# Performance work log

Measured on AMD Instinct MI355X. Metric: run time of the kernel, lower is better.

The kernel has to match this reference:

```python
import jax, jax.numpy as jnp
import numpy as np

B, N, E = 4, 8192, 131072
R, NUM_CLASSES, H, OUT = 16, 100, 128, 32


def _rgcn_layer(h, W, src, dst, rel, mask_edge):
    # h: [B,N,in], W: [R,in,out], src/dst/rel: [B,E] int, mask_edge: [B,E]
    # Per-edge msg = h[src] @ W[rel] * norm(=1); computed as per-relation
    # projection of all nodes followed by a (src, rel) gather.
    proj = jnp.einsum('bni,rio->bnro', h, W)          # [B,N,R,out]
    bidx = jnp.arange(B)[:, None]                      # [B,1]
    msg = proj[bidx, src, rel] * mask_edge[..., None]  # [B,E,out]
    # scatter-sum messages onto destination nodes (fn.sum in DGL)
    seg = (jnp.arange(B)[:, None] * N + dst).reshape(-1)
    out = jax.ops.segment_sum(msg.reshape(B * E, -1), seg, num_segments=B * N)
    return out.reshape(B, N, -1)


def setup_inputs() -> dict:
    key = jax.random.key(0)
    ks = jax.random.split(key, 10)
    class_objects = jax.random.randint(ks[0], (B, N), 0, NUM_CLASSES)
    states_objects = jax.random.normal(ks[1], (B, N, 8), dtype=jnp.float32)
    edge_tuples = jax.random.randint(ks[2], (B, E, 2), 0, N)
    edge_classes = jax.random.randint(ks[3], (B, E), 0, R)
    mask_object = jnp.ones((B, N), dtype=jnp.float32)
    mask_edge = jnp.ones((B, E), dtype=jnp.float32)
    embed = jax.random.normal(ks[4], (NUM_CLASSES, H), dtype=jnp.float32) * 0.05
    W1 = jax.random.normal(ks[5], (R, H, H), dtype=jnp.float32) * 0.05
    W2 = jax.random.normal(ks[6], (R, H, H), dtype=jnp.float32) * 0.05
    W3 = jax.random.normal(ks[7], (R, H, OUT), dtype=jnp.float32) * 0.05
    return {'class_objects': class_objects, 'states_objects': states_objects,
            'edge_tuples': edge_tuples, 'edge_classes': edge_classes,
            'mask_object': mask_object, 'mask_edge': mask_edge,
            'embed': embed, 'W1': W1, 'W2': W2, 'W3': W3}


def reference(class_objects, states_objects, edge_tuples, edge_classes,
              mask_object, mask_edge, embed, W1, W2, W3):
    src = edge_tuples[..., 0]
    dst = edge_tuples[..., 1]
    rel = edge_classes
    h = embed[class_objects]                                  # [B,N,H]
    h = jax.nn.relu(_rgcn_layer(h, W1, src, dst, rel, mask_edge))
    h = jax.nn.relu(_rgcn_layer(h, W2, src, dst, rel, mask_edge))
    h = jax.nn.softmax(_rgcn_layer(h, W3, src, dst, rel, mask_edge), axis=-1)
    # original pads each env's node features with zeros up to max_nodes
    return h * mask_object[..., None]                         # [B,N,OUT]
```

## Files before the change

kernel.cpp:

```cpp
#include <hip/hip_runtime.h>

typedef __attribute__((ext_vector_type(4))) float f32x4;
typedef __attribute__((ext_vector_type(8))) short short8;

#define B_ 4
#define N_ 8192
#define E_ 131072
#define R_ 16
#define H_ 128
#define OUT_ 32
#define NKEYS (B_*N_*R_)
#define NEDGE (B_*E_)
#define NEXT_MASK 0x7FFFFu

__device__ __forceinline__ unsigned short f2bf(float f){
  unsigned int u = __float_as_uint(f);
  u = (u + 0x7fffu + ((u>>16)&1u)) >> 16;
  return (unsigned short)u;
}
__device__ __forceinline__ float bfh(unsigned u, int hi){
  return __uint_as_float(hi ? (u & 0xffff0000u) : (u << 16));
}
__device__ __forceinline__ unsigned cvtpk(float lo, float hi){
  unsigned r;
  asm("v_cvt_pk_bf16_f32 %0, %1, %2" : "=v"(r) : "v"(lo), "v"(hi));
  return r;
}
__device__ __forceinline__ void glds16(const void* g, void* l){
  __builtin_amdgcn_global_load_lds((const __attribute__((address_space(1))) unsigned int*)g,
                                   (__attribute__((address_space(3))) unsigned int*)l,
                                   16, 0, 0);
}


__global__ void link_k(const int* __restrict__ et, const int* __restrict__ ec,
                       int* __restrict__ head, unsigned* __restrict__ link){
  int e = blockIdx.x*256 + threadIdx.x;
  int b = e >> 17;
  int2 sd = *(const int2*)(et + 2*e);
  int r  = ec[e];
  int key = (((b<<13)+sd.y)<<4) + r;
  int old = atomicExch(&head[key], e);
  unsigned nxt = (old < 0) ? (unsigned)e : (unsigned)old;
  link[e] = (((unsigned)sd.x) << 19) | nxt;
}


__global__ void cmap_k(const int* __restrict__ head, const unsigned* __restrict__ link,
                       const float* __restrict__ me,
                       int* __restrict__ cmapA, int* __restrict__ cmapB,
                       int hARow, int hBRow, int aggcRow){
  int key = blockIdx.x*256 + threadIdx.x;
  int hd = head[key];
  int vA = aggcRow, vB = aggcRow;
  if (hd >= 0) {
    unsigned lk = link[hd];
    int nxt = (int)(lk & NEXT_MASK);
    if (nxt == hd && me[hd] == 1.0f) {
      int noderow = ((key >> 17) << 13) + (int)(lk >> 19);
      vA = hARow + noderow;
      vB = hBRow + noderow;
    } else {
      vA = aggcRow + 1 + key;
      vB = vA;
    }
  }
  cmapA[key] = vA;
  cmapB[key] = vB;
}


__global__ void prep_k(const int* __restrict__ cls, const float* __restrict__ emb,
                       const float* __restrict__ W1, const float* __restrict__ W2,
                       const float* __restrict__ W3,
                       unsigned short* __restrict__ h,
                       unsigned short* __restrict__ W1t,
                       unsigned short* __restrict__ W2t,
                       unsigned short* __restrict__ W3t,
                       unsigned short* __restrict__ aggc){
  int t = blockIdx.x*256 + threadIdx.x;
  if (blockIdx.x == 0 && threadIdx.x < 16) {
    *(uint4*)((char*)aggc + threadIdx.x*16) = make_uint4(0,0,0,0);
  }
  if (t < B_*N_*32) {
    int node = t>>5, c = t&31;
    int cl = cls[node];
    float4 v = *(const float4*)(emb + cl*H_ + c*4);
    uint2 o;
    o.x = f2bf(v.x) | ((unsigned int)f2bf(v.y)<<16);
    o.y = f2bf(v.z) | ((unsigned int)f2bf(v.w)<<16);
    *(uint2*)(h + node*H_ + c*4) = o;
  } else {
    int u = t - B_*N_*32;
    if (u < R_*H_*H_) {
      int k = u & 127, n = (u>>7) & 127, r = u >> 14;
      W1t[u] = f2bf(W1[(r*H_ + k)*H_ + n]);
    } else if (u < 2*R_*H_*H_) {
      int u2 = u - R_*H_*H_;
      int k = u2 & 127, n = (u2>>7) & 127, r = u2 >> 14;
      W2t[u2] = f2bf(W2[(r*H_ + k)*H_ + n]);
    } else {
      int u2 = u - 2*R_*H_*H_;
      if (u2 < R_*OUT_*H_) {
        int k = u2 & 127, n = (u2>>7) & 31, r = u2 >> 12;
        W3t[u2] = f2bf(W3[(r*H_ + k)*OUT_ + n]);
      }
    }
  }
}


__global__ __launch_bounds__(256) void agg_k(
    const unsigned short* __restrict__ h_in,
    const int* __restrict__ head,
    const unsigned* __restrict__ link,
    const float* __restrict__ me,
    unsigned short* __restrict__ aggc){
  const int orig = blockIdx.x;
  const int x    = orig & 7;
  const int b    = x >> 1;
  const int lb   = ((x & 1) << 10) + (orig >> 3);
  const int key  = (b << 17) + (lb << 6) + (threadIdx.x >> 2);
  const int q    = threadIdx.x & 3;
  int hd = head[key];
  if (hd < 0) return;
  unsigned lk = link[hd];
  int nxt = (int)(lk & NEXT_MASK);
  float m0 = me[hd];
  if (nxt == hd && m0 == 1.0f) return;
  const unsigned short* hb = h_in + ((size_t)b << 20);

  float fa[32];
  #pragma unroll
  for (int i=0;i<32;++i) fa[i] = 0.f;

#define UNP8(FP, V, M) do { \
  (FP)[0]+=M*bfh((V).x,0); (FP)[1]+=M*bfh((V).x,1); \
  (FP)[2]+=M*bfh((V).y,0); (FP)[3]+=M*bfh((V).y,1); \
  (FP)[4]+=M*bfh((V).z,0); (FP)[5]+=M*bfh((V).z,1); \
  (FP)[6]+=M*bfh((V).w,0); (FP)[7]+=M*bfh((V).w,1); \
} while(0)
#define MAC32(SRC, M) do { \
  const uint4* hp_ = (const uint4*)(hb + (((unsigned)(SRC))<<7) + (q<<5)); \
  uint4 v0_ = hp_[0], v1_ = hp_[1], v2_ = hp_[2], v3_ = hp_[3]; \
  UNP8(fa+0,  v0_, M); UNP8(fa+8,  v1_, M); \
  UNP8(fa+16, v2_, M); UNP8(fa+24, v3_, M); \
} while(0)

  int cur = hd;
  unsigned clk = lk;
  float cm = m0;
  for (;;) {
    int src = (int)(clk >> 19);
    MAC32(src, cm);
    int nx = (int)(clk & NEXT_MASK);
    if (nx == cur) break;
    cur = nx;
    clk = link[cur];
    cm  = me[cur];
  }
#undef MAC32
#undef UNP8

  unsigned short* ap = aggc + (((size_t)(1 + key)) << 7) + (q<<5);
  #pragma unroll
  for (int c = 0; c < 4; ++c) {
    uint4 pk;
    pk.x = cvtpk(fa[c*8+0], fa[c*8+1]);
    pk.y = cvtpk(fa[c*8+2], fa[c*8+3]);
    pk.z = cvtpk(fa[c*8+4], fa[c*8+5]);
    pk.w = cvtpk(fa[c*8+6], fa[c*8+7]);
    *(uint4*)(ap + c*8) = pk;
  }
}


template<int NOUT>
__global__ __launch_bounds__((NOUT==128) ? 1024 : 512, 4) void gemm_k(
    const unsigned short* __restrict__ base,
    const int* __restrict__ cmap,
    const unsigned short* __restrict__ Wt,
    const float* __restrict__ mobj,
    unsigned short* __restrict__ h_out,
    float* __restrict__ out)
{
  constexpr int MT  = (NOUT==128) ? 128 : 64;
  constexpr int MI  = (NOUT==128) ? 2 : 1;
  constexpr int NIw = (NOUT==128) ? 2 : 1;
  __shared__ __align__(16) unsigned short A_s[3][MT*64];
  __shared__ __align__(16) unsigned short B_s[3][NOUT*64];
  __shared__ int cmap_s[MT*16];
  __shared__ float comb[(NOUT==32) ? 64*33 : 1];

  const int tid  = threadIdx.x;
  const int lane = tid & 63;
  const int w    = tid >> 6;
  const int c16  = lane & 15;
  const int g    = lane >> 4;
  const int m0   = blockIdx.x * MT;
  const int mbase = (NOUT==128) ? ((w>>2)<<5) : ((w>>1)<<4);
  const int nbase = (NOUT==128) ? ((w&3)<<5) : ((w&1)<<4);

  *(int2*)&cmap_s[tid<<1] = *(const int2*)(cmap + m0*16 + (tid<<1));
  __syncthreads();

#define STAGE(KC, BUF) do { \
  const int kc_ = (KC); \
  { \
    int m_ = tid>>3, u_ = tid&7; \
    int cm_ = cmap_s[(m_<<4) + (kc_>>1)]; \
    glds16((const char*)base + ((size_t)cm_<<8) + ((kc_&1)<<7) + ((u_ ^ (m_&7))<<4), \
           &A_s[BUF][tid<<3]); \
  } \
  if constexpr (NOUT==128) { \
    int n_ = tid>>3, u_ = tid&7; \
    glds16((const char*)Wt + ((size_t)((kc_>>1)*128 + n_)<<8) + ((kc_&1)<<7) + ((u_ ^ (n_&7))<<4), \
           &B_s[BUF][tid<<3]); \
  } else { \
    if (w < 4) { \
      int uid_ = (w<<6) + lane; \
      int n_ = uid_>>3, u_ = uid_&7; \
      glds16((const char*)Wt + ((size_t)((kc_>>1)*32 + n_)<<8) + ((kc_&1)<<7) + ((u_ ^ (n_&7))<<4), \
             &B_s[BUF][uid_<<3]); } \
  } \
} while(0)

#define WAIT_MAIN do { \
  if constexpr (NOUT==128) { asm volatile("s_waitcnt vmcnt(4)" ::: "memory"); } \
  else { if (w < 4) asm volatile("s_waitcnt vmcnt(4)" ::: "memory"); \
         else       asm volatile("s_waitcnt vmcnt(2)" ::: "memory"); } \
} while(0)
#define WAIT_T1 do { \
  if constexpr (NOUT==128) { asm volatile("s_waitcnt vmcnt(2)" ::: "memory"); } \
  else { if (w < 4) asm volatile("s_waitcnt vmcnt(2)" ::: "memory"); \
         else       asm volatile("s_waitcnt vmcnt(1)" ::: "memory"); } \
} while(0)

  f32x4 acc[MI][NIw];
  #pragma unroll
  for (int mi=0; mi<MI; ++mi)
    #pragma unroll
    for (int ni=0; ni<NIw; ++ni)
      acc[mi][ni] = f32x4{0.f,0.f,0.f,0.f};

#define COMPUTE(BUF) do { \
  _Pragma("unroll") \
  for (int kk=0; kk<2; ++kk) { \
    short8 af[MI], bfr[NIw]; \
    _Pragma("unroll") \
    for (int mi=0; mi<MI; ++mi) { \
      int m_ = mbase + mi*16 + c16; \
      af[mi] = *(const short8*)((const char*)&A_s[BUF][0] + m_*128 \
               + (((kk<<6) + (g<<4)) ^ ((m_&7)<<4))); } \
    _Pragma("unroll") \
    for (int ni=0; ni<NIw; ++ni) { \
      int n_ = nbase + ni*16 + c16; \
      bfr[ni] = *(const short8*)((const char*)&B_s[BUF][0] + n_*128 \
               + (((kk<<6) + (g<<4)) ^ ((n_&7)<<4))); } \
    _Pragma("unroll") \
    for (int mi=0; mi<MI; ++mi) \
      _Pragma("unroll") \
      for (int ni=0; ni<NIw; ++ni) \
        acc[mi][ni] = __builtin_amdgcn_mfma_f32_16x16x32_bf16(af[mi], bfr[ni], acc[mi][ni], 0,0,0); \
  } \
} while(0)

  STAGE(0, 0);
  STAGE(1, 1);
  for (int kc = 0; kc < 30; ++kc) {
    STAGE(kc+2, (kc+2)%3);
    WAIT_MAIN;
    __builtin_amdgcn_s_barrier();
    COMPUTE(kc%3);
    asm volatile("s_waitcnt lgkmcnt(0)" ::: "memory");
    __builtin_amdgcn_s_barrier();
  }
  WAIT_T1;
  __builtin_amdgcn_s_barrier();
  COMPUTE(0);
  asm volatile("s_waitcnt lgkmcnt(0)" ::: "memory");
  __builtin_amdgcn_s_barrier();
  asm volatile("s_waitcnt vmcnt(0)" ::: "memory");
  __builtin_amdgcn_s_barrier();
  COMPUTE(1);

  if constexpr (NOUT == 128) {
    #pragma unroll
    for (int mi=0; mi<MI; ++mi)
      #pragma unroll
      for (int ni=0; ni<NIw; ++ni)
        #pragma unroll
        for (int j=0; j<4; ++j) {
          int row = mbase + mi*16 + (g<<2) + j;
          int col = nbase + ni*16 + c16;
          h_out[((size_t)(m0+row)<<7) + col] = f2bf(fmaxf(acc[mi][ni][j], 0.f));
        }
  } else {
    #pragma unroll
    for (int j=0; j<4; ++j)
      comb[(mbase + (g<<2) + j)*33 + nbase + c16] = acc[0][0][j];
    __syncthreads();
    if (tid < 64) {
      const int row = tid;
      float v[32];
      #pragma unroll
      for (int c=0; c<32; ++c) v[c] = comb[row*33 + c];
      float mx = v[0];
      #pragma unroll
      for (int c=1; c<32; ++c) mx = fmaxf(mx, v[c]);
      float sm = 0.f;
      #pragma unroll
      for (int c=0; c<32; ++c){ v[c] = __expf(v[c]-mx); sm += v[c]; }
      float sc = mobj[m0+row] / sm;
      float4* op = (float4*)(out + ((size_t)(m0+row)<<5));
      #pragma unroll
      for (int c=0; c<8; ++c)
        op[c] = make_float4(v[4*c]*sc, v[4*c+1]*sc, v[4*c+2]*sc, v[4*c+3]*sc);
    }
  }
#undef STAGE
#undef WAIT_MAIN
#undef WAIT_T1
#undef COMPUTE
}

extern "C" void kernel_launch(void* const* d_in, const int* in_sizes, int n_in,
                              void* d_out, int out_size, void* d_ws, size_t ws_size,
                              hipStream_t stream){
  const int*   cls   = (const int*)  d_in[0];
  const int*   et    = (const int*)  d_in[2];
  const int*   ec    = (const int*)  d_in[3];
  const float* mobj  = (const float*)d_in[4];
  const float* medge = (const float*)d_in[5];
  const float* emb   = (const float*)d_in[6];
  const float* W1    = (const float*)d_in[7];
  const float* W2    = (const float*)d_in[8];
  const float* W3    = (const float*)d_in[9];
  float* out = (float*)d_out;

  char* ws = (char*)d_ws;
  size_t o = 0;
  auto alloc = [&](size_t bytes)->char*{
    char* p = ws + o;
    o += (bytes + 255) & ~(size_t)255;
    return p;
  };
  unsigned short* hA    = (unsigned short*)alloc((size_t)B_*N_*H_*2);
  unsigned short* hB    = (unsigned short*)alloc((size_t)B_*N_*H_*2);
  unsigned short* W1t   = (unsigned short*)alloc((size_t)R_*H_*H_*2);
  unsigned short* W2t   = (unsigned short*)alloc((size_t)R_*H_*H_*2);
  unsigned short* W3t   = (unsigned short*)alloc((size_t)R_*OUT_*H_*2);
  int*            head  = (int*)alloc((size_t)NKEYS*4);
  unsigned*       link  = (unsigned*)alloc((size_t)NEDGE*4);
  int*            cmapA = (int*)alloc((size_t)NKEYS*4);
  int*            cmapB = (int*)alloc((size_t)NKEYS*4);
  unsigned short* aggc  = (unsigned short*)alloc(((size_t)NKEYS+1)*H_*2);
  (void)ws_size; (void)in_sizes; (void)n_in; (void)out_size;

  const int hARow   = (int)(((char*)hA   - ws) >> 8);
  const int hBRow   = (int)(((char*)hB   - ws) >> 8);
  const int aggcRow = (int)(((char*)aggc - ws) >> 8);
  const unsigned short* vbase = (const unsigned short*)ws;

  hipMemsetAsync(head, 0xFF, (size_t)NKEYS*4, stream);
  hipLaunchKernelGGL(link_k, dim3(NEDGE/256), dim3(256), 0, stream, et, ec, head, link);
  hipLaunchKernelGGL(cmap_k, dim3(NKEYS/256), dim3(256), 0, stream, head, link, medge,
                     cmapA, cmapB, hARow, hBRow, aggcRow);

  hipLaunchKernelGGL(prep_k, dim3((B_*N_*32 + 2*R_*H_*H_ + R_*OUT_*H_)/256), dim3(256), 0, stream,
                     cls, emb, W1, W2, W3, hA, W1t, W2t, W3t, aggc);

  const int aggGrid = (NKEYS*4)/256;
  const int g128    = (B_*N_)/128;
  const int g32     = (B_*N_)/64;

  hipLaunchKernelGGL(agg_k, dim3(aggGrid), dim3(256), 0, stream, hA, head, link, medge, aggc);
  hipLaunchKernelGGL((gemm_k<128>), dim3(g128), dim3(1024), 0, stream,
                     vbase, cmapA, W1t, (const float*)nullptr, hB, (float*)nullptr);
  hipLaunchKernelGGL(agg_k, dim3(aggGrid), dim3(256), 0, stream, hB, head, link, medge, aggc);
  hipLaunchKernelGGL((gemm_k<128>), dim3(g128), dim3(1024), 0, stream,
                     vbase, cmapB, W2t, (const float*)nullptr, hA, (float*)nullptr);
  hipLaunchKernelGGL(agg_k, dim3(aggGrid), dim3(256), 0, stream, hA, head, link, medge, aggc);
  hipLaunchKernelGGL((gemm_k<32>), dim3(g32), dim3(512), 0, stream,
                     vbase, cmapA, W3t, mobj, (unsigned short*)nullptr, out);
}
```

Baseline: 207.2 us.

## Precompute per-class embedding×W1 table and fuse layer one into edge gather

Layer one's input is an embedding lookup, so each message depends only on the (relation, class) pair. The new code precomputes a 16×100×128 fp32 table of emb·W1[r] and has each node walk its incoming edge lists, summing table rows with relu and bf16 packing fused in. This removes the first aggregation kernel, the first GEMM and the embedding materialisation. In exchange there are serial per-thread linked-list walks with scattered table reads, and accumulation stays in fp32 without the bf16 rounding of h and W1 that the old path applied.

```diff
diff --git a/kernel.cpp b/kernel.cpp
--- a/kernel.cpp
+++ b/kernel.cpp
@@ -9,6 +9,7 @@
 #define R_ 16
 #define H_ 128
 #define OUT_ 32
+#define NCLS 100
 #define NKEYS (B_*N_*R_)
 #define NEDGE (B_*E_)
 #define NEXT_MASK 0x7FFFFu
@@ -70,42 +71,88 @@
 }
 
 
-__global__ void prep_k(const int* __restrict__ cls, const float* __restrict__ emb,
-                       const float* __restrict__ W1, const float* __restrict__ W2,
-                       const float* __restrict__ W3,
-                       unsigned short* __restrict__ h,
-                       unsigned short* __restrict__ W1t,
+__global__ void prep_k(const float* __restrict__ W2, const float* __restrict__ W3,
                        unsigned short* __restrict__ W2t,
                        unsigned short* __restrict__ W3t,
                        unsigned short* __restrict__ aggc){
-  int t = blockIdx.x*256 + threadIdx.x;
+  int u = blockIdx.x*256 + threadIdx.x;
   if (blockIdx.x == 0 && threadIdx.x < 16) {
     *(uint4*)((char*)aggc + threadIdx.x*16) = make_uint4(0,0,0,0);
   }
-  if (t < B_*N_*32) {
-    int node = t>>5, c = t&31;
-    int cl = cls[node];
-    float4 v = *(const float4*)(emb + cl*H_ + c*4);
-    uint2 o;
-    o.x = f2bf(v.x) | ((unsigned int)f2bf(v.y)<<16);
-    o.y = f2bf(v.z) | ((unsigned int)f2bf(v.w)<<16);
-    *(uint2*)(h + node*H_ + c*4) = o;
+  if (u < R_*H_*H_) {
+    int k = u & 127, n = (u>>7) & 127, r = u >> 14;
+    W2t[u] = f2bf(W2[(r*H_ + k)*H_ + n]);
   } else {
-    int u = t - B_*N_*32;
-    if (u < R_*H_*H_) {
-      int k = u & 127, n = (u>>7) & 127, r = u >> 14;
-      W1t[u] = f2bf(W1[(r*H_ + k)*H_ + n]);
-    } else if (u < 2*R_*H_*H_) {
-      int u2 = u - R_*H_*H_;
-      int k = u2 & 127, n = (u2>>7) & 127, r = u2 >> 14;
-      W2t[u2] = f2bf(W2[(r*H_ + k)*H_ + n]);
-    } else {
-      int u2 = u - 2*R_*H_*H_;
-      if (u2 < R_*OUT_*H_) {
-        int k = u2 & 127, n = (u2>>7) & 31, r = u2 >> 12;
-        W3t[u2] = f2bf(W3[(r*H_ + k)*OUT_ + n]);
+    int u2 = u - R_*H_*H_;
+    if (u2 < R_*OUT_*H_) {
+      int k = u2 & 127, n = (u2>>7) & 31, r = u2 >> 12;
+      W3t[u2] = f2bf(W3[(r*H_ + k)*OUT_ + n]);
+    }
+  }
+}
+
+
+__global__ void embw_k(const float* __restrict__ emb, const float* __restrict__ W1,
+                       float* __restrict__ embW1){
+  int t = blockIdx.x*256 + threadIdx.x;
+  int n  = t & 127;
+  int cl = (t >> 7) % NCLS;
+  int r  = t / (NCLS*H_);
+  const float* er = emb + cl*H_;
+  const float* wr = W1 + (size_t)r*H_*H_;
+  float s = 0.f;
+  #pragma unroll 4
+  for (int k = 0; k < H_; ++k)
+    s += er[k] * wr[k*H_ + n];
+  embW1[t] = s;
+}
+
+
+__global__ __launch_bounds__(256) void layer1_k(
+    const int* __restrict__ cls, const float* __restrict__ embW1,
+    const int* __restrict__ head, const unsigned* __restrict__ link,
+    const float* __restrict__ me,
+    unsigned short* __restrict__ h1){
+  int t = blockIdx.x*256 + threadIdx.x;
+  int node = t >> 2;
+  int q = t & 3;
+  const int b = node >> 13;
+  const int* clsb = cls + (b << 13);
+
+  float fa[32];
+  #pragma unroll
+  for (int i=0;i<32;++i) fa[i] = 0.f;
+
+  for (int r = 0; r < R_; ++r) {
+    int cur = head[(node<<4) + r];
+    if (cur < 0) continue;
+    for (;;) {
+      unsigned lk = link[cur];
+      float m = me[cur];
+      int src = (int)(lk >> 19);
+      int cl = clsb[src];
+      const float4* tp = (const float4*)(embW1 + ((r*NCLS + cl) << 7) + (q<<5));
+      #pragma unroll
+      for (int c = 0; c < 8; ++c) {
+        float4 v = tp[c];
+        fa[c*4+0] += m*v.x; fa[c*4+1] += m*v.y;
+        fa[c*4+2] += m*v.z; fa[c*4+3] += m*v.w;
       }
+      int nx = (int)(lk & NEXT_MASK);
+      if (nx == cur) break;
+      cur = nx;
     }
+  }
+
+  unsigned short* op = h1 + ((size_t)node << 7) + (q<<5);
+  #pragma unroll
+  for (int c = 0; c < 4; ++c) {
+    uint4 pk;
+    pk.x = cvtpk(fmaxf(fa[c*8+0],0.f), fmaxf(fa[c*8+1],0.f));
+    pk.y = cvtpk(fmaxf(fa[c*8+2],0.f), fmaxf(fa[c*8+3],0.f));
+    pk.z = cvtpk(fmaxf(fa[c*8+4],0.f), fmaxf(fa[c*8+5],0.f));
+    pk.w = cvtpk(fmaxf(fa[c*8+6],0.f), fmaxf(fa[c*8+7],0.f));
+    *(uint4*)(op + c*8) = pk;
   }
 }
 
@@ -347,7 +394,7 @@
   };
   unsigned short* hA    = (unsigned short*)alloc((size_t)B_*N_*H_*2);
   unsigned short* hB    = (unsigned short*)alloc((size_t)B_*N_*H_*2);
-  unsigned short* W1t   = (unsigned short*)alloc((size_t)R_*H_*H_*2);
+  float*          embW1 = (float*)alloc((size_t)R_*NCLS*H_*4);
   unsigned short* W2t   = (unsigned short*)alloc((size_t)R_*H_*H_*2);
   unsigned short* W3t   = (unsigned short*)alloc((size_t)R_*OUT_*H_*2);
   int*            head  = (int*)alloc((size_t)NKEYS*4);
@@ -367,16 +414,16 @@
   hipLaunchKernelGGL(cmap_k, dim3(NKEYS/256), dim3(256), 0, stream, head, link, medge,
                      cmapA, cmapB, hARow, hBRow, aggcRow);
 
-  hipLaunchKernelGGL(prep_k, dim3((B_*N_*32 + 2*R_*H_*H_ + R_*OUT_*H_)/256), dim3(256), 0, stream,
-                     cls, emb, W1, W2, W3, hA, W1t, W2t, W3t, aggc);
+  hipLaunchKernelGGL(prep_k, dim3((R_*H_*H_ + R_*OUT_*H_)/256), dim3(256), 0, stream,
+                     W2, W3, W2t, W3t, aggc);
+  hipLaunchKernelGGL(embw_k, dim3(R_*NCLS*H_/256), dim3(256), 0, stream, emb, W1, embW1);
 
   const int aggGrid = (NKEYS*4)/256;
   const int g128    = (B_*N_)/128;
   const int g32     = (B_*N_)/64;
 
-  hipLaunchKernelGGL(agg_k, dim3(aggGrid), dim3(256), 0, stream, hA, head, link, medge, aggc);
-  hipLaunchKernelGGL((gemm_k<128>), dim3(g128), dim3(1024), 0, stream,
-                     vbase, cmapA, W1t, (const float*)nullptr, hB, (float*)nullptr);
+  hipLaunchKernelGGL(layer1_k, dim3(B_*N_*4/256), dim3(256), 0, stream,
+                     cls, embW1, head, link, medge, hB);
   hipLaunchKernelGGL(agg_k, dim3(aggGrid), dim3(256), 0, stream, hB, head, link, medge, aggc);
   hipLaunchKernelGGL((gemm_k<128>), dim3(g128), dim3(1024), 0, stream,
                      vbase, cmapB, W2t, (const float*)nullptr, hA, (float*)nullptr);
```

Result: slower. 236.5 us (+14.2%).
